# Kernel optimization log

Hardware: AMD Instinct MI355X
Metric: run time of the kernel (lower is better)

The kernel has to match this reference:

```python
import math
import jax, jax.numpy as jnp
import numpy as np

EMBED_DIM = 1024
NUM_HEADS = 16
HEAD_DIM = EMBED_DIM // NUM_HEADS


def setup_inputs() -> dict:
    key = jax.random.key(0)
    k1, k2, k3, k4 = jax.random.split(key, 4)
    B, S = 4, 2048
    x = jax.random.normal(k1, (B, S, EMBED_DIM), dtype=jnp.float32)
    mask = jnp.ones((B, S), dtype=jnp.int32)  # key-padding mask, 1 = keep
    # nn.Linear(embed_dim, 3*embed_dim, bias=False): weight [3E, E]
    w_qkv = jax.random.normal(k2, (3 * EMBED_DIM, EMBED_DIM), dtype=jnp.float32) / math.sqrt(EMBED_DIM)
    # nn.Linear(embed_dim, embed_dim): weight [E, E], bias [E]
    w_out = jax.random.normal(k3, (EMBED_DIM, EMBED_DIM), dtype=jnp.float32) / math.sqrt(EMBED_DIM)
    b_out = jax.random.normal(k4, (EMBED_DIM,), dtype=jnp.float32) * 0.01
    return {"x": x, "w_qkv": w_qkv, "w_out": w_out, "b_out": b_out, "mask": mask}


def _attention(x, w_qkv, w_out, b_out, mask):
    B, S, E = x.shape
    qkv = jnp.einsum("bse,fe->bsf", x, w_qkv)  # [B,S,3E]
    q, k, v = jnp.split(qkv, 3, axis=-1)
    def heads(t):  # [B,S,E] -> [B,H,S,D]
        return t.reshape(B, S, NUM_HEADS, HEAD_DIM).transpose(0, 2, 1, 3)
    q, k, v = heads(q), heads(k), heads(v)
    scores = jnp.einsum("bhqd,bhkd->bhqk", q, k) / math.sqrt(HEAD_DIM)
    keep = (mask != 0)[:, None, None, :]  # [B,1,1,S]
    scores = jnp.where(keep, scores, jnp.float32(-1e9))
    probs = jax.nn.softmax(scores, axis=-1)
    # dropout p=0.0 -> identity (eval semantics)
    out = jnp.einsum("bhqk,bhkd->bhqd", probs, v)
    out = out.transpose(0, 2, 1, 3).reshape(B, S, E)
    return jnp.einsum("bse,fe->bsf", out, w_out) + b_out


def reference(x, w_qkv, w_out, b_out, mask):
    return _attention(x, w_qkv, w_out, b_out, mask)
```

## Files before the change

### kernel.cpp

```cpp
#include <hip/hip_runtime.h>

#define EMB 1024
#define NH 16
#define HD 64
#define SEQ 2048
#define BB 4

typedef __attribute__((ext_vector_type(8))) short bf8;
typedef __attribute__((ext_vector_type(4))) short bf4;
typedef __attribute__((ext_vector_type(4))) float f4;

#define MFMA16(a, b, c) __builtin_amdgcn_mfma_f32_16x16x32_bf16((a), (b), (c), 0, 0, 0)

#if defined(__has_builtin)
#if __has_builtin(__builtin_amdgcn_mfma_f32_16x16x16_bf16_1k)
#define HAVE_MFMA16X16 1
#endif
#if __has_builtin(__builtin_amdgcn_exp2f)
#define EXP2F __builtin_amdgcn_exp2f
#endif
#if __has_builtin(__builtin_amdgcn_cvt_pk_bf16_f32)
#define HAVE_PK_BF16 1
#endif
#if __has_builtin(__builtin_amdgcn_perm)
#define HAVE_PERM 1
#endif
#endif
#ifndef EXP2F
#define EXP2F exp2f
#endif

__device__ inline f4 pv_mfma(bf4 a, bf4 b, f4 c) {
#ifdef HAVE_MFMA16X16
  return __builtin_amdgcn_mfma_f32_16x16x16_bf16_1k(a, b, c, 0, 0, 0);
#else
  bf8 av, bv;
  *(bf4*)&av = a;  ((int*)&av)[2] = 0; ((int*)&av)[3] = 0;
  *(bf4*)&bv = b;  ((int*)&bv)[2] = 0; ((int*)&bv)[3] = 0;
  return __builtin_amdgcn_mfma_f32_16x16x32_bf16(av, bv, c, 0, 0, 0);
#endif
}

#define GLL16(g, l)                                                     \
  __builtin_amdgcn_global_load_lds(                                     \
      (__attribute__((address_space(1))) void*)(g),                     \
      (__attribute__((address_space(3))) void*)(l), 16, 0, 0)

__device__ inline unsigned short f2bf(float f) {
  union { float f; unsigned u; } v; v.f = f;
  unsigned u = v.u;
  u += 0x7fffu + ((u >> 16) & 1u);
  return (unsigned short)(u >> 16);
}

__device__ inline unsigned pkbf(float a, float b) {
#ifdef HAVE_PK_BF16
  typedef __attribute__((ext_vector_type(2))) __bf16 bf16x2;
  union { bf16x2 v; unsigned u; } c;
  c.v = __builtin_amdgcn_cvt_pk_bf16_f32(a, b);
  return c.u;
#elif defined(HAVE_PERM)
  union { float f; unsigned u; } ua, ub; ua.f = a; ub.f = b;
  return __builtin_amdgcn_perm(ub.u + 0x8000u, ua.u + 0x8000u, 0x07060302u);
#else
  union { float f; unsigned u; } ua, ub; ua.f = a; ub.f = b;
  return ((ua.u + 0x8000u) >> 16) | ((ub.u + 0x8000u) & 0xFFFF0000u);
#endif
}

__global__ void cvt_all(const float* __restrict__ x, const float* __restrict__ wq,
                        const float* __restrict__ wo, unsigned short* __restrict__ out) {
  int i = blockIdx.x * blockDim.x + threadIdx.x;
  float4 f;
  if (i < 2097152)      f = ((const float4*)x)[i];
  else if (i < 2883584) f = ((const float4*)wq)[i - 2097152];
  else                  f = ((const float4*)wo)[i - 2883584];
  ushort4 o;
  o.x = f2bf(f.x); o.y = f2bf(f.y); o.z = f2bf(f.z); o.w = f2bf(f.w);
  ((ushort4*)out)[i] = o;
}

template <bool OUTF32>
__global__ __launch_bounds__(256, 2) void gemm_bt(
    const unsigned short* __restrict__ A, const unsigned short* __restrict__ B,
    void* __restrict__ Cout, const float* __restrict__ bias,
    unsigned short* __restrict__ vtb,
    int M, int N, int K, int ldC, int nsplit) {
  __shared__ unsigned short la[128 * 32];
  __shared__ unsigned short lb[128 * 32];

  const int t = threadIdx.x;
  const int lane = t & 63;
  const int w = t >> 6;
  const int quad = lane >> 4;
  const int lcol = lane & 15;
  const int m0 = blockIdx.y * 128;
  const int n0 = blockIdx.x * 128;
  const int wm = (w & 1) * 64;
  const int wn = (w >> 1) * 64;

  f4 acc[4][4];
#pragma unroll
  for (int i = 0; i < 4; i++)
#pragma unroll
    for (int j = 0; j < 4; j++) acc[i][j] = (f4){0.f, 0.f, 0.f, 0.f};

  const int srow = t >> 2;
  const int scol = (t & 3) * 8;
  const unsigned short* gA = A + (size_t)(m0 + srow) * K + scol;
  const unsigned short* gB = B + (size_t)(n0 + srow) * K + scol;
  unsigned short* lA = la + t * 8;
  unsigned short* lB = lb + t * 8;

  for (int kt = 0; kt < K; kt += 32) {
    __syncthreads();
    GLL16(gA + kt, lA);
    GLL16(gA + kt + (size_t)64 * K, lA + 64 * 32);
    GLL16(gB + kt, lB);
    GLL16(gB + kt + (size_t)64 * K, lB + 64 * 32);
    __syncthreads();

    bf8 af[4], bfr[4];
#pragma unroll
    for (int i = 0; i < 4; i++) {
      af[i]  = *(const bf8*)&la[(wm + i * 16 + lcol) * 32 + quad * 8];
      bfr[i] = *(const bf8*)&lb[(wn + i * 16 + lcol) * 32 + quad * 8];
    }
#pragma unroll
    for (int i = 0; i < 4; i++)
#pragma unroll
      for (int j = 0; j < 4; j++)
        acc[i][j] = MFMA16(af[i], bfr[j], acc[i][j]);
  }

  if (!OUTF32 && n0 >= nsplit) {
#pragma unroll
    for (int i = 0; i < 4; i++) {
#pragma unroll
      for (int j = 0; j < 4; j++) {
        int f = n0 + wn + j * 16 + lcol - nsplit;
        int mg = m0 + wm + i * 16 + quad * 4;
        int bb = mg >> 11, ss = mg & 2047;
        ushort4 pk;
        pk.x = f2bf(acc[i][j][0]); pk.y = f2bf(acc[i][j][1]);
        pk.z = f2bf(acc[i][j][2]); pk.w = f2bf(acc[i][j][3]);
        *(ushort4*)&vtb[((size_t)(bb * 1024 + f)) * 2048 + ss] = pk;
      }
    }
  } else {
#pragma unroll
    for (int i = 0; i < 4; i++) {
#pragma unroll
      for (int j = 0; j < 4; j++) {
#pragma unroll
        for (int r = 0; r < 4; r++) {
          int m = m0 + wm + i * 16 + quad * 4 + r;
          int n = n0 + wn + j * 16 + lcol;
          if (OUTF32) {
            float v = acc[i][j][r] + (bias ? bias[n] : 0.f);
            ((float*)Cout)[(size_t)m * ldC + n] = v;
          } else {
            ((unsigned short*)Cout)[(size_t)m * ldC + n] = f2bf(acc[i][j][r]);
          }
        }
      }
    }
  }
}

#define SCALE_LOG2E 0.1803368801111244f
#define BKEEP (-16.0f / SCALE_LOG2E)
#define BDROP (-1e30f / SCALE_LOG2E)

__global__ __launch_bounds__(512, 4) void attn_kernel(
    const unsigned short* __restrict__ qk, const unsigned short* __restrict__ vtg,
    const int* __restrict__ mask, unsigned short* __restrict__ outb) {
  __shared__ unsigned short kv[2 * 16384];
  __shared__ __align__(16) float bt[2][128];

  const int t = threadIdx.x;
  const int lane = t & 63;
  const int w = t >> 6;
  const int quad = lane >> 4;
  const int lcol = lane & 15;
  const int lx = lcol & 7;

  const int id = blockIdx.x + (blockIdx.y << 4) + (blockIdx.z << 8);
  const int g  = (id & 7) + ((id >> 7) << 3);
  const int q0 = ((id >> 3) & 15) * 128;
  const int h = g & 15;
  const int b = g >> 4;

  const unsigned short* qbase = qk + (size_t)(b * SEQ) * 2048 + h * HD;
  const unsigned short* kbase = qbase + 1024;
  const unsigned short* vbase = vtg + (size_t)((b * 16 + h) * 64) * SEQ;

  const int qrow = q0 + w * 16 + lcol;
  const bf8 qf0 = *(const bf8*)(qbase + (size_t)qrow * 2048 + quad * 8);
  const bf8 qf1 = *(const bf8*)(qbase + (size_t)qrow * 2048 + 32 + quad * 8);

  f4 o[4];
#pragma unroll
  for (int db = 0; db < 4; db++) o[db] = (f4){0.f, 0.f, 0.f, 0.f};
  float lsum = 0.f;

  const int sr = t >> 3;
  const int sc = ((t & 7) ^ (sr & 7)) * 8;
  const unsigned short* gk = kbase + (size_t)sr * 2048 + sc;
  const int vd = t >> 4;
  const int vc8 = ((t & 15) ^ (vd & 7)) * 8;
  const unsigned short* gv = vbase + (size_t)vd * SEQ + vc8;

  const int NT = SEQ / 128;

  GLL16(gk, kv + t * 8);
  GLL16(gk + (size_t)64 * 2048, kv + 4096 + t * 8);
  GLL16(gv, kv + 8192 + t * 8);
  GLL16(gv + (size_t)32 * SEQ, kv + 12288 + t * 8);
  if (t < 128) bt[0][t] = mask[b * SEQ + t] ? BKEEP : BDROP;
  int pmv = (t < 128) ? mask[b * SEQ + 128 + t] : 0;

  for (int it = 0; it < NT; ++it) {
    const int cur = (it & 1) * 16384;
    __syncthreads();

    if (it + 1 < NT) {
      const int nxt = ((it + 1) & 1) * 16384;
      const size_t k1 = (size_t)(it + 1) * 128;
      GLL16(gk + k1 * 2048, kv + nxt + t * 8);
      GLL16(gk + (k1 + 64) * 2048, kv + nxt + 4096 + t * 8);
      GLL16(gv + k1, kv + nxt + 8192 + t * 8);
      GLL16(gv + (size_t)32 * SEQ + k1, kv + nxt + 12288 + t * 8);
      if (t < 128) bt[(it + 1) & 1][t] = pmv ? BKEEP : BDROP;
      int kn = (it + 2 < NT) ? (it + 2) * 128 : 0;
      pmv = (t < 128) ? mask[b * SEQ + kn + t] : 0;
    }

    const unsigned short* kcur = kv + cur;
    const unsigned short* vcur = kv + cur + 8192;
    const float* bcur = bt[it & 1];

#pragma unroll
    for (int hh = 0; hh < 2; hh++) {
      f4 sT[4];
      __builtin_amdgcn_s_setprio(1);
#pragma unroll
      for (int kb = 0; kb < 4; kb++) {
        const unsigned short* krow = kcur + (hh * 64 + kb * 16 + lcol) * 64;
        bf8 kf0 = *(const bf8*)&krow[(quad ^ lx) * 8];
        bf8 kf1 = *(const bf8*)&krow[((4 + quad) ^ lx) * 8];
        f4 a = *(const f4*)&bcur[hh * 64 + kb * 16 + quad * 4];
        a = MFMA16(kf0, qf0, a);
        a = MFMA16(kf1, qf1, a);
        sT[kb] = a;
      }
      __builtin_amdgcn_s_setprio(0);

      bf4 pfrag[4];
#pragma unroll
      for (int kb = 0; kb < 4; kb++) {
        float p0 = EXP2F(sT[kb][0] * SCALE_LOG2E);
        float p1 = EXP2F(sT[kb][1] * SCALE_LOG2E);
        float p2 = EXP2F(sT[kb][2] * SCALE_LOG2E);
        float p3 = EXP2F(sT[kb][3] * SCALE_LOG2E);
        lsum += (p0 + p1) + (p2 + p3);
        union { unsigned u[2]; bf4 s; } cv;
        cv.u[0] = pkbf(p0, p1);
        cv.u[1] = pkbf(p2, p3);
        pfrag[kb] = cv.s;
      }

      __builtin_amdgcn_s_setprio(1);
#pragma unroll
      for (int db = 0; db < 4; db++) {
        const unsigned short* vrow = vcur + (db * 16 + lcol) * 128;
#pragma unroll
        for (int kb = 0; kb < 4; kb++) {
          int c = ((hh * 4 + kb) << 1) | (quad >> 1);
          bf4 vf = *(const bf4*)&vrow[(c ^ lx) * 8 + (quad & 1) * 4];
          o[db] = pv_mfma(vf, pfrag[kb], o[db]);
        }
      }
      __builtin_amdgcn_s_setprio(0);
    }
  }

  lsum += __shfl_xor(lsum, 16);
  lsum += __shfl_xor(lsum, 32);
  float inv = 1.f / lsum;
#pragma unroll
  for (int db = 0; db < 4; db++) {
    ushort4 pk;
    pk.x = f2bf(o[db][0] * inv);
    pk.y = f2bf(o[db][1] * inv);
    pk.z = f2bf(o[db][2] * inv);
    pk.w = f2bf(o[db][3] * inv);
    *(ushort4*)&outb[(size_t)(b * SEQ + q0 + w * 16 + lcol) * EMB + h * HD +
                     db * 16 + quad * 4] = pk;
  }
}

extern "C" void kernel_launch(void* const* d_in, const int* in_sizes, int n_in,
                              void* d_out, int out_size, void* d_ws, size_t ws_size,
                              hipStream_t stream) {
  const float* x     = (const float*)d_in[0];
  const float* w_qkv = (const float*)d_in[1];
  const float* w_out = (const float*)d_in[2];
  const float* b_out = (const float*)d_in[3];
  const int*   mask  = (const int*)d_in[4];

  char* ws = (char*)d_ws;
  unsigned short* xb    = (unsigned short*)(ws + 0);
  unsigned short* wqkvb = (unsigned short*)(ws + 16777216);
  unsigned short* woutb = (unsigned short*)(ws + 23068672);
  unsigned short* qkb   = (unsigned short*)(ws + 25165824);
  unsigned short* attnb = (unsigned short*)(ws + 58720256);
  unsigned short* vtb   = (unsigned short*)(ws + 75497472);

  cvt_all<<<12288, 256, 0, stream>>>(x, w_qkv, w_out, (unsigned short*)ws);

  gemm_bt<false><<<dim3(24, 64), 256, 0, stream>>>(
      xb, wqkvb, (void*)qkb, nullptr, vtb, 8192, 3072, 1024, 2048, 2048);

  attn_kernel<<<dim3(16, 16, 4), 512, 0, stream>>>(qkb, vtb, mask, attnb);

  gemm_bt<true><<<dim3(8, 64), 256, 0, stream>>>(
      attnb, woutb, d_out, b_out, nullptr, 8192, 1024, 1024, 1024, 1 << 30);
}
```

Baseline: 312.5 us.

## Process two 16-row query tiles per wave in attention to reuse K/V fragments

Each wave now handles 32 query rows (two 16-row sub-tiles) instead of 16, so each block covers 256 queries and the grid is halved. Every K and V fragment read from LDS feeds two MFMAs, which halves LDS traffic and global K/V loads per query. The cost is double the accumulator and probability registers, which may lower occupancy under the 512x4 launch bounds, and only 512 blocks are launched.

```diff
diff --git a/kernel.cpp b/kernel.cpp
--- a/kernel.cpp
+++ b/kernel.cpp
@@ -185,9 +185,9 @@
   const int lcol = lane & 15;
   const int lx = lcol & 7;
 
-  const int id = blockIdx.x + (blockIdx.y << 4) + (blockIdx.z << 8);
-  const int g  = (id & 7) + ((id >> 7) << 3);
-  const int q0 = ((id >> 3) & 15) * 128;
+  const int id = blockIdx.x + (blockIdx.y << 3) + (blockIdx.z << 7);
+  const int g  = (id & 7) | ((id >> 6) << 3);
+  const int q0 = ((id >> 3) & 7) * 256;
   const int h = g & 15;
   const int b = g >> 4;
 
@@ -195,14 +195,20 @@
   const unsigned short* kbase = qbase + 1024;
   const unsigned short* vbase = vtg + (size_t)((b * 16 + h) * 64) * SEQ;
 
-  const int qrow = q0 + w * 16 + lcol;
-  const bf8 qf0 = *(const bf8*)(qbase + (size_t)qrow * 2048 + quad * 8);
-  const bf8 qf1 = *(const bf8*)(qbase + (size_t)qrow * 2048 + 32 + quad * 8);
-
-  f4 o[4];
-#pragma unroll
-  for (int db = 0; db < 4; db++) o[db] = (f4){0.f, 0.f, 0.f, 0.f};
-  float lsum = 0.f;
+  const int qrA = q0 + w * 32 + lcol;
+  const int qrB = qrA + 16;
+  const bf8 qf0A = *(const bf8*)(qbase + (size_t)qrA * 2048 + quad * 8);
+  const bf8 qf1A = *(const bf8*)(qbase + (size_t)qrA * 2048 + 32 + quad * 8);
+  const bf8 qf0B = *(const bf8*)(qbase + (size_t)qrB * 2048 + quad * 8);
+  const bf8 qf1B = *(const bf8*)(qbase + (size_t)qrB * 2048 + 32 + quad * 8);
+
+  f4 oA[4], oB[4];
+#pragma unroll
+  for (int db = 0; db < 4; db++) {
+    oA[db] = (f4){0.f, 0.f, 0.f, 0.f};
+    oB[db] = (f4){0.f, 0.f, 0.f, 0.f};
+  }
+  float lsumA = 0.f, lsumB = 0.f;
 
   const int sr = t >> 3;
   const int sc = ((t & 7) ^ (sr & 7)) * 8;
@@ -242,32 +248,44 @@
 
 #pragma unroll
     for (int hh = 0; hh < 2; hh++) {
-      f4 sT[4];
+      f4 sTA[4], sTB[4];
       __builtin_amdgcn_s_setprio(1);
 #pragma unroll
       for (int kb = 0; kb < 4; kb++) {
         const unsigned short* krow = kcur + (hh * 64 + kb * 16 + lcol) * 64;
         bf8 kf0 = *(const bf8*)&krow[(quad ^ lx) * 8];
         bf8 kf1 = *(const bf8*)&krow[((4 + quad) ^ lx) * 8];
-        f4 a = *(const f4*)&bcur[hh * 64 + kb * 16 + quad * 4];
-        a = MFMA16(kf0, qf0, a);
-        a = MFMA16(kf1, qf1, a);
-        sT[kb] = a;
+        f4 ab = *(const f4*)&bcur[hh * 64 + kb * 16 + quad * 4];
+        f4 aA = MFMA16(kf0, qf0A, ab);
+        aA = MFMA16(kf1, qf1A, aA);
+        sTA[kb] = aA;
+        f4 aB = MFMA16(kf0, qf0B, ab);
+        aB = MFMA16(kf1, qf1B, aB);
+        sTB[kb] = aB;
       }
       __builtin_amdgcn_s_setprio(0);
 
-      bf4 pfrag[4];
+      bf4 pfragA[4], pfragB[4];
 #pragma unroll
       for (int kb = 0; kb < 4; kb++) {
-        float p0 = EXP2F(sT[kb][0] * SCALE_LOG2E);
-        float p1 = EXP2F(sT[kb][1] * SCALE_LOG2E);
-        float p2 = EXP2F(sT[kb][2] * SCALE_LOG2E);
-        float p3 = EXP2F(sT[kb][3] * SCALE_LOG2E);
-        lsum += (p0 + p1) + (p2 + p3);
-        union { unsigned u[2]; bf4 s; } cv;
-        cv.u[0] = pkbf(p0, p1);
-        cv.u[1] = pkbf(p2, p3);
-        pfrag[kb] = cv.s;
+        float a0 = EXP2F(sTA[kb][0] * SCALE_LOG2E);
+        float a1 = EXP2F(sTA[kb][1] * SCALE_LOG2E);
+        float a2 = EXP2F(sTA[kb][2] * SCALE_LOG2E);
+        float a3 = EXP2F(sTA[kb][3] * SCALE_LOG2E);
+        lsumA += (a0 + a1) + (a2 + a3);
+        union { unsigned u[2]; bf4 s; } ca;
+        ca.u[0] = pkbf(a0, a1);
+        ca.u[1] = pkbf(a2, a3);
+        pfragA[kb] = ca.s;
+        float b0 = EXP2F(sTB[kb][0] * SCALE_LOG2E);
+        float b1 = EXP2F(sTB[kb][1] * SCALE_LOG2E);
+        float b2 = EXP2F(sTB[kb][2] * SCALE_LOG2E);
+        float b3 = EXP2F(sTB[kb][3] * SCALE_LOG2E);
+        lsumB += (b0 + b1) + (b2 + b3);
+        union { unsigned u[2]; bf4 s; } cb;
+        cb.u[0] = pkbf(b0, b1);
+        cb.u[1] = pkbf(b2, b3);
+        pfragB[kb] = cb.s;
       }
 
       __builtin_amdgcn_s_setprio(1);
@@ -278,25 +296,36 @@
         for (int kb = 0; kb < 4; kb++) {
           int c = ((hh * 4 + kb) << 1) | (quad >> 1);
           bf4 vf = *(const bf4*)&vrow[(c ^ lx) * 8 + (quad & 1) * 4];
-          o[db] = pv_mfma(vf, pfrag[kb], o[db]);
+          oA[db] = pv_mfma(vf, pfragA[kb], oA[db]);
+          oB[db] = pv_mfma(vf, pfragB[kb], oB[db]);
         }
       }
       __builtin_amdgcn_s_setprio(0);
     }
   }
 
-  lsum += __shfl_xor(lsum, 16);
-  lsum += __shfl_xor(lsum, 32);
-  float inv = 1.f / lsum;
+  lsumA += __shfl_xor(lsumA, 16);
+  lsumA += __shfl_xor(lsumA, 32);
+  lsumB += __shfl_xor(lsumB, 16);
+  lsumB += __shfl_xor(lsumB, 32);
+  float invA = 1.f / lsumA;
+  float invB = 1.f / lsumB;
 #pragma unroll
   for (int db = 0; db < 4; db++) {
     ushort4 pk;
-    pk.x = f2bf(o[db][0] * inv);
-    pk.y = f2bf(o[db][1] * inv);
-    pk.z = f2bf(o[db][2] * inv);
-    pk.w = f2bf(o[db][3] * inv);
-    *(ushort4*)&outb[(size_t)(b * SEQ + q0 + w * 16 + lcol) * EMB + h * HD +
+    pk.x = f2bf(oA[db][0] * invA);
+    pk.y = f2bf(oA[db][1] * invA);
+    pk.z = f2bf(oA[db][2] * invA);
+    pk.w = f2bf(oA[db][3] * invA);
+    *(ushort4*)&outb[(size_t)(b * SEQ + qrA) * EMB + h * HD +
                      db * 16 + quad * 4] = pk;
+    ushort4 pk2;
+    pk2.x = f2bf(oB[db][0] * invB);
+    pk2.y = f2bf(oB[db][1] * invB);
+    pk2.z = f2bf(oB[db][2] * invB);
+    pk2.w = f2bf(oB[db][3] * invB);
+    *(ushort4*)&outb[(size_t)(b * SEQ + qrB) * EMB + h * HD +
+                     db * 16 + quad * 4] = pk2;
   }
 }
 
@@ -322,7 +351,7 @@
   gemm_bt<false><<<dim3(24, 64), 256, 0, stream>>>(
       xb, wqkvb, (void*)qkb, nullptr, vtb, 8192, 3072, 1024, 2048, 2048);
 
-  attn_kernel<<<dim3(16, 16, 4), 512, 0, stream>>>(qkb, vtb, mask, attnb);
+  attn_kernel<<<dim3(8, 16, 4), 512, 0, stream>>>(qkb, vtb, mask, attnb);
 
   gemm_bt<true><<<dim3(8, 64), 256, 0, stream>>>(
       attnb, woutb, d_out, b_out, nullptr, 8192, 1024, 1024, 1024, 1 << 30);
```

Result: slower. 735.8 us (+135.4%).
